# Kernel optimization log

Measured on AMD Instinct MI355X. Metric: run time of the kernel, lower is better.

The kernel has to match this reference:

```python
import jax, jax.numpy as jnp
import numpy as np

B, S, D, H = 2, 2048, 1024, 16
DH = D // H
EPS = 1e-5
NEG = -1e9


def layer_norm(x, scale, bias):
    mu = jnp.mean(x, axis=-1, keepdims=True)
    var = jnp.mean((x - mu) ** 2, axis=-1, keepdims=True)
    return (x - mu) * jax.lax.rsqrt(var + EPS) * scale + bias


def setup_inputs() -> dict:
    key = jax.random.key(0)
    ks = jax.random.split(key, 8)
    scale = 1.0 / np.sqrt(D)
    x = jax.random.normal(ks[0], (B, S, D), dtype=jnp.float32)
    padding_mask = jnp.ones((B, S), dtype=bool)
    # per-head QKV projections stacked over heads: (H, D, DH)
    Wq = jax.random.normal(ks[1], (H, D, DH), dtype=jnp.float32) * scale
    Wk = jax.random.normal(ks[2], (H, D, DH), dtype=jnp.float32) * scale
    Wv = jax.random.normal(ks[3], (H, D, DH), dtype=jnp.float32) * scale
    ln1_s = jnp.ones((D,), jnp.float32); ln1_b = jnp.zeros((D,), jnp.float32)
    ln2_s = jnp.ones((D,), jnp.float32); ln2_b = jnp.zeros((D,), jnp.float32)
    W1 = jax.random.normal(ks[4], (D, D), dtype=jnp.float32) * scale
    b1 = jnp.zeros((D,), jnp.float32)
    W2 = jax.random.normal(ks[5], (D, D), dtype=jnp.float32) * scale
    b2 = jnp.zeros((D,), jnp.float32)
    return dict(x=x, padding_mask=padding_mask, Wq=Wq, Wk=Wk, Wv=Wv,
                ln1_s=ln1_s, ln1_b=ln1_b, ln2_s=ln2_s, ln2_b=ln2_b,
                W1=W1, b1=b1, W2=W2, b2=b2)


def reference(x, padding_mask, Wq, Wk, Wv, ln1_s, ln1_b, ln2_s, ln2_b, W1, b1, W2, b2):
    # pre-norm attention with residual (dropout = identity at eval)
    h = layer_norm(x, ln1_s, ln1_b)
    q = jnp.einsum('bsd,hde->bhse', h, Wq)
    k = jnp.einsum('bsd,hde->bhse', h, Wk)
    v = jnp.einsum('bsd,hde->bhse', h, Wv)
    scores = jnp.einsum('bhse,bhte->bhst', q, k) / jnp.sqrt(jnp.float32(DH))
    causal = jnp.tril(jnp.ones((S, S), dtype=bool))           # (S,S)
    mask = padding_mask[:, None, None, :] & causal[None, None]  # (B,1,S,S)
    scores = jnp.where(mask, scores, NEG)
    p = jax.nn.softmax(scores, axis=-1)
    z = jnp.einsum('bhst,bhte->bshe', p, v).reshape(x.shape[0], x.shape[1], D)
    x = x + z
    # pre-norm FFN with residual
    h2 = layer_norm(x, ln2_s, ln2_b)
    ff = jax.nn.relu(h2 @ W1 + b1) @ W2 + b2
    return x + ff
```

## Files before the change

### kernel.cpp

```cpp
#include <hip/hip_runtime.h>
#include <hip/hip_bf16.h>
#include <stdint.h>

#define NB 2
#define NS 2048
#define ND 1024
#define NH 16
#define NDH 64
#define NT (NB*NS)

using f32x4  = __attribute__((ext_vector_type(4))) float;
using bf16x8 = __attribute__((ext_vector_type(8))) short;
using uint2v = __attribute__((ext_vector_type(2))) unsigned int;

typedef __attribute__((address_space(1))) unsigned int as1_uint;
typedef __attribute__((address_space(3))) unsigned int as3_uint;

__device__ __forceinline__ void llds16(void* l, const void* g) {
    __builtin_amdgcn_global_load_lds((as1_uint*)g, (as3_uint*)l, 16, 0, 0);
}

__device__ __forceinline__ f32x4 mfma16(bf16x8 a, bf16x8 b, f32x4 c) {
    return __builtin_amdgcn_mfma_f32_16x16x32_bf16(a, b, c, 0, 0, 0);
}

__device__ __forceinline__ unsigned short f2bf(float f) {
    union { __hip_bfloat16 h; unsigned short u; } cv;
    cv.h = __float2bfloat16(f);
    return cv.u;
}

__device__ __forceinline__ float fmax_x16(float v) {
    uint2v r = __builtin_amdgcn_permlane16_swap(__float_as_uint(v), __float_as_uint(v), false, false);
    return fmaxf(__uint_as_float(r.x), __uint_as_float(r.y));
}
__device__ __forceinline__ float fmax_x32(float v) {
    uint2v r = __builtin_amdgcn_permlane32_swap(__float_as_uint(v), __float_as_uint(v), false, false);
    return fmaxf(__uint_as_float(r.x), __uint_as_float(r.y));
}
__device__ __forceinline__ float fadd_x16(float v) {
    uint2v r = __builtin_amdgcn_permlane16_swap(__float_as_uint(v), __float_as_uint(v), false, false);
    return __uint_as_float(r.x) + __uint_as_float(r.y);
}
__device__ __forceinline__ float fadd_x32(float v) {
    uint2v r = __builtin_amdgcn_permlane32_swap(__float_as_uint(v), __float_as_uint(v), false, false);
    return __uint_as_float(r.x) + __uint_as_float(r.y);
}

__global__ void k_prep(const float* __restrict__ Wq, const float* __restrict__ Wk,
                       const float* __restrict__ Wv, const float* __restrict__ W1,
                       const float* __restrict__ W2, unsigned short* __restrict__ WcatT,
                       unsigned short* __restrict__ W1T, unsigned short* __restrict__ W2T) {
    __shared__ float tile[64][65];
    int tid = threadIdx.x;
    int bid = blockIdx.x;
    if (bid < 768) {
        const float SCALEQ = 0.125f * 1.44269504088896f;
        int kt = bid & 15; bid >>= 4;
        int h  = bid & 15; bid >>= 4;
        int mat = bid;
        const float* W = (mat == 0) ? Wq : (mat == 1) ? Wk : Wv;
#pragma unroll
        for (int i = 0; i < 16; ++i) {
            int idx = tid + i * 256;
            int r = idx >> 6, e = idx & 63;
            tile[r][e] = W[(size_t)h * ND * NDH + (size_t)(kt * 64 + r) * NDH + e];
        }
        __syncthreads();
#pragma unroll
        for (int i = 0; i < 16; ++i) {
            int idx = tid + i * 256;
            int e = idx >> 6, r = idx & 63;
            float v = tile[r][e];
            if (mat == 0) v *= SCALEQ;
            WcatT[(size_t)(mat * 1024 + h * 64 + e) * ND + kt * 64 + r] = f2bf(v);
        }
    } else {
        const float* W = (bid < 1024) ? W1 : W2;
        unsigned short* WT = (bid < 1024) ? W1T : W2T;
        int lb = (bid - 768) & 255;
        int ntile = lb & 15;
        int ktile = lb >> 4;
#pragma unroll
        for (int i = 0; i < 16; ++i) {
            int idx = tid + i * 256;
            int r = idx >> 6, c = idx & 63;
            tile[r][c] = W[(size_t)(ktile * 64 + r) * ND + ntile * 64 + c];
        }
        __syncthreads();
#pragma unroll
        for (int i = 0; i < 16; ++i) {
            int idx = tid + i * 256;
            int c = idx >> 6, r = idx & 63;
            WT[(size_t)(ntile * 64 + c) * ND + ktile * 64 + r] = f2bf(tile[r][c]);
        }
    }
}

__global__ void k_ln(const float* __restrict__ x, const float* __restrict__ sc,
                     const float* __restrict__ bi, unsigned short* __restrict__ out) {
    int row = blockIdx.x;
    int tid = threadIdx.x;
    const float* xr = x + (size_t)row * ND;
    float4 v = reinterpret_cast<const float4*>(xr)[tid];
    float sum = v.x + v.y + v.z + v.w;
    float sq  = v.x * v.x + v.y * v.y + v.z * v.z + v.w * v.w;
#pragma unroll
    for (int off = 1; off < 64; off <<= 1) {
        sum += __shfl_xor(sum, off);
        sq  += __shfl_xor(sq, off);
    }
    __shared__ float ssum[4], ssq[4];
    int wave = tid >> 6;
    if ((tid & 63) == 0) { ssum[wave] = sum; ssq[wave] = sq; }
    __syncthreads();
    sum = ssum[0] + ssum[1] + ssum[2] + ssum[3];
    sq  = ssq[0] + ssq[1] + ssq[2] + ssq[3];
    float mu  = sum * (1.0f / ND);
    float var = sq * (1.0f / ND) - mu * mu;
    float rstd = rsqrtf(var + 1e-5f);
    float4 s4 = reinterpret_cast<const float4*>(sc)[tid];
    float4 b4 = reinterpret_cast<const float4*>(bi)[tid];
    ushort4 o;
    o.x = f2bf((v.x - mu) * rstd * s4.x + b4.x);
    o.y = f2bf((v.y - mu) * rstd * s4.y + b4.y);
    o.z = f2bf((v.z - mu) * rstd * s4.z + b4.z);
    o.w = f2bf((v.w - mu) * rstd * s4.w + b4.w);
    reinterpret_cast<ushort4*>(out + (size_t)row * ND)[tid] = o;
}

template<bool BIAS, bool RELU, bool RES>
__global__ __launch_bounds__(256)
void k_gemm(const unsigned short* __restrict__ A, const unsigned short* __restrict__ Bt,
            const float* __restrict__ bias, const float* __restrict__ res,
            void* __restrict__ Cv, int N, int K) {
    __shared__ __align__(16) unsigned short As[2][64 * 64];
    __shared__ __align__(16) unsigned short Bs[2][128 * 64];
    int tid = threadIdx.x;
    int lane = tid & 63, wave = tid >> 6;
    int wm = wave >> 1, wn = wave & 1;
    int l16 = lane & 15, lg = lane >> 4;
    int ntiles = N >> 7;
    int wg = (blockIdx.x & 7) * (gridDim.x >> 3) + (blockIdx.x >> 3);
    int mt = wg / ntiles;
    int nt = wg % ntiles;

    const unsigned short* Abase = A  + (size_t)(mt * 64) * K;
    const unsigned short* Bbase = Bt + (size_t)(nt * 128) * K;

    f32x4 acc[2][4];
#pragma unroll
    for (int i = 0; i < 2; ++i)
#pragma unroll
        for (int j = 0; j < 4; ++j) acc[i][j] = (f32x4){0.f, 0.f, 0.f, 0.f};

    int srow = tid >> 3;
    int sch  = tid & 7;
    int KT = K >> 6;

    auto STAGE = [&](int kt, int bufi) {
#pragma unroll
        for (int i = 0; i < 2; ++i) {
            int row = srow + i * 32;
            int cs = sch ^ (row & 7);
            llds16((char*)As[bufi] + wave * 1024 + i * 4096,
                   Abase + (size_t)row * K + kt * 64 + cs * 8);
        }
#pragma unroll
        for (int i = 0; i < 4; ++i) {
            int row = srow + i * 32;
            int cs = sch ^ (row & 7);
            llds16((char*)Bs[bufi] + wave * 1024 + i * 4096,
                   Bbase + (size_t)row * K + kt * 64 + cs * 8);
        }
    };

    STAGE(0, 0);
    for (int kt = 0; kt < KT; ++kt) {
        int cb = kt & 1;
        if (kt + 1 < KT) {
            STAGE(kt + 1, cb ^ 1);
            asm volatile("s_waitcnt vmcnt(6)" ::: "memory");
        } else {
            asm volatile("s_waitcnt vmcnt(0)" ::: "memory");
        }
        __builtin_amdgcn_s_barrier();

        bf16x8 af[2][2], bfb[4][2];
#pragma unroll
        for (int mi = 0; mi < 2; ++mi)
#pragma unroll
            for (int kc = 0; kc < 2; ++kc) {
                int row = wm * 32 + mi * 16 + l16;
                int ch = (kc * 4 + lg) ^ (row & 7);
                af[mi][kc] = *reinterpret_cast<const bf16x8*>((const char*)As[cb] + row * 128 + ch * 16);
            }
#pragma unroll
        for (int ni = 0; ni < 4; ++ni)
#pragma unroll
            for (int kc = 0; kc < 2; ++kc) {
                int row = wn * 64 + ni * 16 + l16;
                int ch = (kc * 4 + lg) ^ (row & 7);
                bfb[ni][kc] = *reinterpret_cast<const bf16x8*>((const char*)Bs[cb] + row * 128 + ch * 16);
            }
#pragma unroll
        for (int mi = 0; mi < 2; ++mi)
#pragma unroll
            for (int ni = 0; ni < 4; ++ni) {
                acc[mi][ni] = mfma16(af[mi][0], bfb[ni][0], acc[mi][ni]);
                acc[mi][ni] = mfma16(af[mi][1], bfb[ni][1], acc[mi][ni]);
            }
        __builtin_amdgcn_s_barrier();
    }

#pragma unroll
    for (int mi = 0; mi < 2; ++mi)
#pragma unroll
        for (int ni = 0; ni < 4; ++ni) {
            int col = nt * 128 + wn * 64 + ni * 16 + l16;
            float bv = BIAS ? bias[col] : 0.f;
#pragma unroll
            for (int r = 0; r < 4; ++r) {
                int row = mt * 64 + wm * 32 + mi * 16 + lg * 4 + r;
                float v = acc[mi][ni][r] + bv;
                if (RELU) v = fmaxf(v, 0.f);
                size_t idx = (size_t)row * N + col;
                if (RES) ((float*)Cv)[idx] = v + res[idx];
                else ((unsigned short*)Cv)[idx] = f2bf(v);
            }
        }
}

__global__ __launch_bounds__(256)
void k_attn(const unsigned short* __restrict__ qk, const unsigned short* __restrict__ VT,
            const float* __restrict__ x, float* __restrict__ x2) {
    constexpr int ldq = 2 * ND;
    int bid = blockIdx.x;
    int c  = bid & 255;
    int g  = bid >> 8;
    int s  = c >> 5;
    int bh = c & 31;
    int qb = (g == 0) ? 31 - s : (g == 1) ? 16 + s : (g == 2) ? 15 - s : s;
    int h = bh & 15, b = bh >> 4;
    int tid = threadIdx.x;
    int lane = tid & 63, wave = tid >> 6;
    int l16 = lane & 15, lg = lane >> 4;

    const unsigned short* Qp = qk + (size_t)b * NS * ldq + h * NDH;
    const unsigned short* Kp = Qp + ND;
    const unsigned short* Vp = VT + (size_t)(h * NDH) * NT + b * NS;

    __shared__ __align__(16) unsigned short Ks[2][64 * 64];
    __shared__ __align__(16) unsigned short Vs[2][64 * 64];
    __shared__ __align__(16) unsigned short Ps[4][16 * 64];

    int srow = tid >> 3;
    int sch  = tid & 7;

    int nt = qb + 1;
    int qw = qb * 64 + wave * 16;

    bf16x8 qf[2];
#pragma unroll
    for (int kc = 0; kc < 2; ++kc)
        qf[kc] = *reinterpret_cast<const bf16x8*>(Qp + (size_t)(qw + l16) * ldq + kc * 32 + lg * 8);

    f32x4 oacc[4];
#pragma unroll
    for (int i = 0; i < 4; ++i) oacc[i] = (f32x4){0.f, 0.f, 0.f, 0.f};
    float m_run = -1.0e30f, l_part = 0.0f;

    char* pbase = (char*)&Ps[wave][0] + l16 * 128;
    int psw = l16 & 7;

#pragma unroll
    for (int i = 0; i < 2; ++i) {
        int row = srow + i * 32;
        int cs = sch ^ (row & 7);
        llds16((char*)Ks[0] + wave * 1024 + i * 4096, Kp + (size_t)row * ldq + cs * 8);
    }
#pragma unroll
    for (int i = 0; i < 2; ++i) {
        int row = srow + i * 32;
        int cs = sch ^ (row & 7);
        llds16((char*)Vs[0] + wave * 1024 + i * 4096, Vp + (size_t)row * NT + cs * 8);
    }

    for (int t = 0; t < nt; ++t) {
        int cur = t & 1;
        const char* Kcur = (const char*)Ks[cur];
        const char* Vcur = (const char*)Vs[cur];

        if (t + 1 < nt) {
#pragma unroll
            for (int i = 0; i < 2; ++i) {
                int row = srow + i * 32;
                int cs = sch ^ (row & 7);
                llds16((char*)Ks[cur ^ 1] + wave * 1024 + i * 4096,
                       Kp + (size_t)((t + 1) * 64 + row) * ldq + cs * 8);
            }
#pragma unroll
            for (int i = 0; i < 2; ++i) {
                int row = srow + i * 32;
                int cs = sch ^ (row & 7);
                llds16((char*)Vs[cur ^ 1] + wave * 1024 + i * 4096,
                       Vp + (size_t)row * NT + (t + 1) * 64 + cs * 8);
            }
            asm volatile("s_waitcnt vmcnt(4)" ::: "memory");
        } else {
            asm volatile("s_waitcnt vmcnt(0)" ::: "memory");
        }
        __builtin_amdgcn_s_barrier();

        f32x4 st[4];
#pragma unroll
        for (int mtt = 0; mtt < 4; ++mtt) st[mtt] = (f32x4){0.f, 0.f, 0.f, 0.f};
        __builtin_amdgcn_s_setprio(1);
#pragma unroll
        for (int kc = 0; kc < 2; ++kc)
#pragma unroll
            for (int mtt = 0; mtt < 4; ++mtt) {
                int row = mtt * 16 + l16;
                int ch = (kc * 4 + lg) ^ (row & 7);
                bf16x8 kf = *reinterpret_cast<const bf16x8*>(Kcur + row * 128 + ch * 16);
                st[mtt] = mfma16(kf, qf[kc], st[mtt]);
            }
        __builtin_amdgcn_s_setprio(0);

        float sv[4][4];
        float mx = -3.0e38f;
        if (t == qb) {
            int qg = qw + l16;
#pragma unroll
            for (int mtt = 0; mtt < 4; ++mtt)
#pragma unroll
                for (int r = 0; r < 4; ++r) {
                    int key = t * 64 + mtt * 16 + lg * 4 + r;
                    float s2 = (key <= qg) ? st[mtt][r] : -1.0e30f;
                    sv[mtt][r] = s2;
                    mx = fmaxf(mx, s2);
                }
        } else {
#pragma unroll
            for (int mtt = 0; mtt < 4; ++mtt)
#pragma unroll
                for (int r = 0; r < 4; ++r) {
                    float s2 = st[mtt][r];
                    sv[mtt][r] = s2;
                    mx = fmaxf(mx, s2);
                }
        }
        mx = fmax_x16(mx);
        mx = fmax_x32(mx);

        if (__ballot(mx > m_run + 8.0f)) {
            float mnew = fmaxf(m_run, mx);
            float alpha = exp2f(m_run - mnew);
            m_run = mnew;
            l_part *= alpha;
#pragma unroll
            for (int r = 0; r < 4; ++r) {
                float ar = __shfl(alpha, (lane & 48) | (lg * 4 + r));
#pragma unroll
                for (int ntt = 0; ntt < 4; ++ntt) oacc[ntt][r] *= ar;
            }
        }

#pragma unroll
        for (int mtt = 0; mtt < 4; ++mtt) {
            float p0 = exp2f(sv[mtt][0] - m_run);
            float p1 = exp2f(sv[mtt][1] - m_run);
            float p2 = exp2f(sv[mtt][2] - m_run);
            float p3 = exp2f(sv[mtt][3] - m_run);
            l_part += (p0 + p1) + (p2 + p3);
            int b0 = mtt * 32 + lg * 8;
            int sb = ((((b0 >> 4) ^ psw) << 4) | (b0 & 15));
            uint2 u;
            u.x = (unsigned)f2bf(p0) | ((unsigned)f2bf(p1) << 16);
            u.y = (unsigned)f2bf(p2) | ((unsigned)f2bf(p3) << 16);
            *reinterpret_cast<uint2*>(pbase + sb) = u;
        }

        asm volatile("s_waitcnt lgkmcnt(0)" ::: "memory");

        __builtin_amdgcn_s_setprio(1);
#pragma unroll
        for (int kc = 0; kc < 2; ++kc) {
            bf16x8 pa = *reinterpret_cast<const bf16x8*>(pbase + (((kc * 4 + lg) ^ psw) << 4));
#pragma unroll
            for (int ntt = 0; ntt < 4; ++ntt) {
                int vrow = ntt * 16 + l16;
                bf16x8 vb = *reinterpret_cast<const bf16x8*>(
                    Vcur + vrow * 128 + ((((kc * 4 + lg) ^ (vrow & 7)) << 4)));
                oacc[ntt] = mfma16(pa, vb, oacc[ntt]);
            }
        }
        __builtin_amdgcn_s_setprio(0);
        __builtin_amdgcn_s_barrier();
    }

    float l_run = fadd_x32(fadd_x16(l_part));
#pragma unroll
    for (int r = 0; r < 4; ++r) {
        float lv = __shfl(l_run, (lane & 48) | (lg * 4 + r));
        float linv = 1.0f / lv;
        int tkn = b * NS + qw + lg * 4 + r;
        size_t base = (size_t)tkn * ND + h * NDH;
#pragma unroll
        for (int ntt = 0; ntt < 4; ++ntt) {
            size_t idx = base + ntt * 16 + l16;
            x2[idx] = x[idx] + oacc[ntt][r] * linv;
        }
    }
}

extern "C" void kernel_launch(void* const* d_in, const int* in_sizes, int n_in,
                              void* d_out, int out_size, void* d_ws, size_t ws_size,
                              hipStream_t stream) {
    const float* x    = (const float*)d_in[0];
    const float* Wq   = (const float*)d_in[2];
    const float* Wk   = (const float*)d_in[3];
    const float* Wv   = (const float*)d_in[4];
    const float* ln1s = (const float*)d_in[5];
    const float* ln1b = (const float*)d_in[6];
    const float* ln2s = (const float*)d_in[7];
    const float* ln2b = (const float*)d_in[8];
    const float* W1   = (const float*)d_in[9];
    const float* b1   = (const float*)d_in[10];
    const float* W2   = (const float*)d_in[11];
    const float* b2   = (const float*)d_in[12];
    float* out = (float*)d_out;

    char* ws = (char*)d_ws;
    unsigned short* WcatT = (unsigned short*)(ws);
    unsigned short* W1T   = (unsigned short*)(ws + 6291456);
    unsigned short* W2T   = (unsigned short*)(ws + 8388608);
    unsigned short* hbuf  = (unsigned short*)(ws + 10485760);
    unsigned short* qkbuf = (unsigned short*)(ws + 18874368);
    unsigned short* vtbuf = (unsigned short*)(ws + 35651584);
    float*          x2    = (float*)(ws + 44040192);
    unsigned short* ubuf  = qkbuf;

    k_prep<<<1280, 256, 0, stream>>>(Wq, Wk, Wv, W1, W2, WcatT, W1T, W2T);
    k_ln<<<NT, 256, 0, stream>>>(x, ln1s, ln1b, hbuf);
    k_gemm<false, false, false><<<(NT / 64) * (2048 / 128), 256, 0, stream>>>(
        hbuf, WcatT, nullptr, nullptr, qkbuf, 2048, 1024);
    k_gemm<false, false, false><<<(1024 / 64) * (NT / 128), 256, 0, stream>>>(
        WcatT + (size_t)2048 * 1024, hbuf, nullptr, nullptr, vtbuf, NT, 1024);
    k_attn<<<NB * NH * 32, 256, 0, stream>>>(qkbuf, vtbuf, x, x2);
    k_ln<<<NT, 256, 0, stream>>>(x2, ln2s, ln2b, hbuf);
    k_gemm<true, true, false><<<(NT / 64) * (1024 / 128), 256, 0, stream>>>(
        hbuf, W1T, b1, nullptr, ubuf, 1024, 1024);
    k_gemm<true, false, true><<<(NT / 64) * (1024 / 128), 256, 0, stream>>>(
        ubuf, W2T, b2, x2, out, 1024, 1024);
}
```

Baseline: 149.6 us.

## Merge prep with LN1, fuse QK and V GEMMs, load V directly to registers

Folds the weight-prep kernel and the first layernorm into one launch, and runs the QK and V^T projection GEMMs as a single dual-grid launch, cutting launch gaps and tail idle time. In attention, V tiles are no longer staged through LDS. Each lane loads its MFMA B-operand fragments straight from global memory into registers, with vmcnt waits retuned and the barrier moved to sit after the QK MFMAs. This frees LDS and removes LDS traffic for V, at the cost of uncoalesced 16-byte global loads and more registers.

```diff
diff --git a/kernel.cpp b/kernel.cpp
--- a/kernel.cpp
+++ b/kernel.cpp
@@ -47,11 +47,14 @@
     return __uint_as_float(r.x) + __uint_as_float(r.y);
 }
 
-__global__ void k_prep(const float* __restrict__ Wq, const float* __restrict__ Wk,
-                       const float* __restrict__ Wv, const float* __restrict__ W1,
-                       const float* __restrict__ W2, unsigned short* __restrict__ WcatT,
-                       unsigned short* __restrict__ W1T, unsigned short* __restrict__ W2T) {
+__global__ void k_prep_ln(const float* __restrict__ Wq, const float* __restrict__ Wk,
+                          const float* __restrict__ Wv, const float* __restrict__ W1,
+                          const float* __restrict__ W2, unsigned short* __restrict__ WcatT,
+                          unsigned short* __restrict__ W1T, unsigned short* __restrict__ W2T,
+                          const float* __restrict__ x, const float* __restrict__ sc,
+                          const float* __restrict__ bi, unsigned short* __restrict__ hout) {
     __shared__ float tile[64][65];
+    __shared__ float ssum[4], ssq[4];
     int tid = threadIdx.x;
     int bid = blockIdx.x;
     if (bid < 768) {
@@ -75,7 +78,7 @@
             if (mat == 0) v *= SCALEQ;
             WcatT[(size_t)(mat * 1024 + h * 64 + e) * ND + kt * 64 + r] = f2bf(v);
         }
-    } else {
+    } else if (bid < 1280) {
         const float* W = (bid < 1024) ? W1 : W2;
         unsigned short* WT = (bid < 1024) ? W1T : W2T;
         int lb = (bid - 768) & 255;
@@ -94,6 +97,33 @@
             int c = idx >> 6, r = idx & 63;
             WT[(size_t)(ntile * 64 + c) * ND + ktile * 64 + r] = f2bf(tile[r][c]);
         }
+    } else {
+        int row = bid - 1280;
+        const float* xr = x + (size_t)row * ND;
+        float4 v = reinterpret_cast<const float4*>(xr)[tid];
+        float sum = v.x + v.y + v.z + v.w;
+        float sq  = v.x * v.x + v.y * v.y + v.z * v.z + v.w * v.w;
+#pragma unroll
+        for (int off = 1; off < 64; off <<= 1) {
+            sum += __shfl_xor(sum, off);
+            sq  += __shfl_xor(sq, off);
+        }
+        int wave = tid >> 6;
+        if ((tid & 63) == 0) { ssum[wave] = sum; ssq[wave] = sq; }
+        __syncthreads();
+        sum = ssum[0] + ssum[1] + ssum[2] + ssum[3];
+        sq  = ssq[0] + ssq[1] + ssq[2] + ssq[3];
+        float mu  = sum * (1.0f / ND);
+        float var = sq * (1.0f / ND) - mu * mu;
+        float rstd = rsqrtf(var + 1e-5f);
+        float4 s4 = reinterpret_cast<const float4*>(sc)[tid];
+        float4 b4 = reinterpret_cast<const float4*>(bi)[tid];
+        ushort4 o;
+        o.x = f2bf((v.x - mu) * rstd * s4.x + b4.x);
+        o.y = f2bf((v.y - mu) * rstd * s4.y + b4.y);
+        o.z = f2bf((v.z - mu) * rstd * s4.z + b4.z);
+        o.w = f2bf((v.w - mu) * rstd * s4.w + b4.w);
+        reinterpret_cast<ushort4*>(hout + (size_t)row * ND)[tid] = o;
     }
 }
 
@@ -130,10 +160,10 @@
 }
 
 template<bool BIAS, bool RELU, bool RES>
-__global__ __launch_bounds__(256)
-void k_gemm(const unsigned short* __restrict__ A, const unsigned short* __restrict__ Bt,
-            const float* __restrict__ bias, const float* __restrict__ res,
-            void* __restrict__ Cv, int N, int K) {
+__device__ __forceinline__
+void gemm_core(const unsigned short* __restrict__ A, const unsigned short* __restrict__ Bt,
+               const float* __restrict__ bias, const float* __restrict__ res,
+               void* __restrict__ Cv, int N, int K, int wg) {
     __shared__ __align__(16) unsigned short As[2][64 * 64];
     __shared__ __align__(16) unsigned short Bs[2][128 * 64];
     int tid = threadIdx.x;
@@ -141,7 +171,6 @@
     int wm = wave >> 1, wn = wave & 1;
     int l16 = lane & 15, lg = lane >> 4;
     int ntiles = N >> 7;
-    int wg = (blockIdx.x & 7) * (gridDim.x >> 3) + (blockIdx.x >> 3);
     int mt = wg / ntiles;
     int nt = wg % ntiles;
 
@@ -229,6 +258,32 @@
                 else ((unsigned short*)Cv)[idx] = f2bf(v);
             }
         }
+}
+
+template<bool BIAS, bool RELU, bool RES>
+__global__ __launch_bounds__(256)
+void k_gemm(const unsigned short* __restrict__ A, const unsigned short* __restrict__ Bt,
+            const float* __restrict__ bias, const float* __restrict__ res,
+            void* __restrict__ Cv, int N, int K) {
+    int wg = (blockIdx.x & 7) * (gridDim.x >> 3) + (blockIdx.x >> 3);
+    gemm_core<BIAS, RELU, RES>(A, Bt, bias, res, Cv, N, K, wg);
+}
+
+__global__ __launch_bounds__(256)
+void k_gemm_dual(const unsigned short* __restrict__ A0, const unsigned short* __restrict__ Bt0,
+                 void* __restrict__ C0, int N0,
+                 const unsigned short* __restrict__ A1, const unsigned short* __restrict__ Bt1,
+                 void* __restrict__ C1, int N1, int K, int split) {
+    int bid = blockIdx.x;
+    if (bid < split) {
+        int wg = (bid & 7) * (split >> 3) + (bid >> 3);
+        gemm_core<false, false, false>(A0, Bt0, nullptr, nullptr, C0, N0, K, wg);
+    } else {
+        int lb = bid - split;
+        int nblk = gridDim.x - split;
+        int wg = (lb & 7) * (nblk >> 3) + (lb >> 3);
+        gemm_core<false, false, false>(A1, Bt1, nullptr, nullptr, C1, N1, K, wg);
+    }
 }
 
 __global__ __launch_bounds__(256)
@@ -251,7 +306,6 @@
     const unsigned short* Vp = VT + (size_t)(h * NDH) * NT + b * NS;
 
     __shared__ __align__(16) unsigned short Ks[2][64 * 64];
-    __shared__ __align__(16) unsigned short Vs[2][64 * 64];
     __shared__ __align__(16) unsigned short Ps[4][16 * 64];
 
     int srow = tid >> 3;
@@ -272,6 +326,8 @@
 
     char* pbase = (char*)&Ps[wave][0] + l16 * 128;
     int psw = l16 & 7;
+
+    const unsigned short* vrow = Vp + (size_t)l16 * NT + lg * 8;
 
 #pragma unroll
     for (int i = 0; i < 2; ++i) {
@@ -279,18 +335,18 @@
         int cs = sch ^ (row & 7);
         llds16((char*)Ks[0] + wave * 1024 + i * 4096, Kp + (size_t)row * ldq + cs * 8);
     }
-#pragma unroll
-    for (int i = 0; i < 2; ++i) {
-        int row = srow + i * 32;
-        int cs = sch ^ (row & 7);
-        llds16((char*)Vs[0] + wave * 1024 + i * 4096, Vp + (size_t)row * NT + cs * 8);
-    }
 
     for (int t = 0; t < nt; ++t) {
         int cur = t & 1;
         const char* Kcur = (const char*)Ks[cur];
-        const char* Vcur = (const char*)Vs[cur];
-
+
+        bf16x8 vreg[8];
+#pragma unroll
+        for (int ntt = 0; ntt < 4; ++ntt) {
+            const unsigned short* p = vrow + (size_t)(ntt * 16) * NT + t * 64;
+            vreg[ntt * 2 + 0] = *reinterpret_cast<const bf16x8*>(p);
+            vreg[ntt * 2 + 1] = *reinterpret_cast<const bf16x8*>(p + 32);
+        }
         if (t + 1 < nt) {
 #pragma unroll
             for (int i = 0; i < 2; ++i) {
@@ -299,16 +355,9 @@
                 llds16((char*)Ks[cur ^ 1] + wave * 1024 + i * 4096,
                        Kp + (size_t)((t + 1) * 64 + row) * ldq + cs * 8);
             }
-#pragma unroll
-            for (int i = 0; i < 2; ++i) {
-                int row = srow + i * 32;
-                int cs = sch ^ (row & 7);
-                llds16((char*)Vs[cur ^ 1] + wave * 1024 + i * 4096,
-                       Vp + (size_t)row * NT + (t + 1) * 64 + cs * 8);
-            }
-            asm volatile("s_waitcnt vmcnt(4)" ::: "memory");
+            asm volatile("s_waitcnt vmcnt(10)" ::: "memory");
         } else {
-            asm volatile("s_waitcnt vmcnt(0)" ::: "memory");
+            asm volatile("s_waitcnt vmcnt(8)" ::: "memory");
         }
         __builtin_amdgcn_s_barrier();
 
@@ -326,6 +375,7 @@
                 st[mtt] = mfma16(kf, qf[kc], st[mtt]);
             }
         __builtin_amdgcn_s_setprio(0);
+        __builtin_amdgcn_s_barrier();
 
         float sv[4][4];
         float mx = -3.0e38f;
@@ -382,6 +432,11 @@
         }
 
         asm volatile("s_waitcnt lgkmcnt(0)" ::: "memory");
+        if (t + 1 < nt) {
+            asm volatile("s_waitcnt vmcnt(2)" ::: "memory");
+        } else {
+            asm volatile("s_waitcnt vmcnt(0)" ::: "memory");
+        }
 
         __builtin_amdgcn_s_setprio(1);
 #pragma unroll
@@ -389,14 +444,10 @@
             bf16x8 pa = *reinterpret_cast<const bf16x8*>(pbase + (((kc * 4 + lg) ^ psw) << 4));
 #pragma unroll
             for (int ntt = 0; ntt < 4; ++ntt) {
-                int vrow = ntt * 16 + l16;
-                bf16x8 vb = *reinterpret_cast<const bf16x8*>(
-                    Vcur + vrow * 128 + ((((kc * 4 + lg) ^ (vrow & 7)) << 4)));
-                oacc[ntt] = mfma16(pa, vb, oacc[ntt]);
+                oacc[ntt] = mfma16(pa, vreg[ntt * 2 + kc], oacc[ntt]);
             }
         }
         __builtin_amdgcn_s_setprio(0);
-        __builtin_amdgcn_s_barrier();
     }
 
     float l_run = fadd_x32(fadd_x16(l_part));
@@ -441,12 +492,11 @@
     float*          x2    = (float*)(ws + 44040192);
     unsigned short* ubuf  = qkbuf;
 
-    k_prep<<<1280, 256, 0, stream>>>(Wq, Wk, Wv, W1, W2, WcatT, W1T, W2T);
-    k_ln<<<NT, 256, 0, stream>>>(x, ln1s, ln1b, hbuf);
-    k_gemm<false, false, false><<<(NT / 64) * (2048 / 128), 256, 0, stream>>>(
-        hbuf, WcatT, nullptr, nullptr, qkbuf, 2048, 1024);
-    k_gemm<false, false, false><<<(1024 / 64) * (NT / 128), 256, 0, stream>>>(
-        WcatT + (size_t)2048 * 1024, hbuf, nullptr, nullptr, vtbuf, NT, 1024);
+    k_prep_ln<<<1280 + NT, 256, 0, stream>>>(Wq, Wk, Wv, W1, W2, WcatT, W1T, W2T,
+                                             x, ln1s, ln1b, hbuf);
+    k_gemm_dual<<<1024 + 512, 256, 0, stream>>>(
+        hbuf, WcatT, qkbuf, 2048,
+        WcatT + (size_t)2048 * 1024, hbuf, vtbuf, NT, 1024, 1024);
     k_attn<<<NB * NH * 32, 256, 0, stream>>>(qkbuf, vtbuf, x, x2);
     k_ln<<<NT, 256, 0, stream>>>(x2, ln2s, ln2b, hbuf);
     k_gemm<true, true, false><<<(NT / 64) * (1024 / 128), 256, 0, stream>>>(
```

Result: slower. 168.6 us (+12.7%).
